# Optimization experiments

Measured on AMD Instinct MI355X. Metric: run time of the kernel, lower is better.

## Reference

```python
import jax, jax.numpy as jnp
from jax import lax
import numpy as np

B, T, D, H = 32, 512, 512, 1024  # batch, n_steps, in_channels (embedding), cell units


def setup_inputs() -> dict:
    key = jax.random.key(0)
    k1, k2, k3, k4 = jax.random.split(key, 4)
    inputs = jax.random.normal(k1, (B, T, D), dtype=jnp.float32)
    # actual (unpadded) length of each sequence, in [1, T]
    sequence_length = jax.random.randint(k2, (B,), 1, T + 1).astype(jnp.int32)
    # LSTMCell params: kernel [D, 4H], recurrent_kernel [H, 4H], bias [4H]; gate order i,f,g,o
    Wx = jax.random.normal(k3, (D, 4 * H), dtype=jnp.float32) * (1.0 / np.sqrt(D))
    Wh = jax.random.normal(k4, (H, 4 * H), dtype=jnp.float32) * (1.0 / np.sqrt(H))
    # unit_forget_bias=True: forget-gate bias initialized to 1
    b = jnp.concatenate([jnp.zeros((H,)), jnp.ones((H,)), jnp.zeros((2 * H,))]).astype(jnp.float32)
    return {"inputs": inputs, "sequence_length": sequence_length, "Wx": Wx, "Wh": Wh, "b": b}


def _lstm_all_outputs(inputs, Wx, Wh, b):
    # Precompute input projections for every timestep (big batched GEMM, fused).
    x_proj = jnp.einsum('btd,dk->btk', inputs, Wx) + b  # [B, T, 4H]

    def step(carry, xz_t):
        h, c = carry
        z = xz_t + h @ Wh  # [B, 4H]
        i, f, g, o = jnp.split(z, 4, axis=-1)
        i = jax.nn.sigmoid(i)
        f = jax.nn.sigmoid(f)
        o = jax.nn.sigmoid(o)
        c = f * c + i * jnp.tanh(g)
        h = o * jnp.tanh(c)
        return (h, c), h

    h0 = jnp.zeros((inputs.shape[0], Wh.shape[0]), dtype=inputs.dtype)
    c0 = h0
    (_, _), hs = lax.scan(step, (h0, c0), jnp.swapaxes(x_proj, 0, 1))  # hs: [T, B, H]
    return jnp.swapaxes(hs, 0, 1)  # [B, T, H]


def reference(inputs, sequence_length, Wx, Wh, b):
    # return_last_output=True with sequence_length: gather the output at the
    # actual last valid timestep (seq_len - 1) of each sequence.
    hs = _lstm_all_outputs(inputs, Wx, Wh, b)  # [B, T, H]
    last_idx = jnp.clip(sequence_length - 1, 0, inputs.shape[1] - 1)
    return hs[jnp.arange(hs.shape[0]), last_idx]  # [B, H]
```

## Files before the change

### kernel.cpp

```cpp
#include <hip/hip_runtime.h>
#include <hip/hip_bf16.h>


#define B_   32
#define T_   512
#define D_   512
#define H_   1024
#define KTOT 1536
#define N4H  4096
#define NBLK 64

typedef __bf16 bf16_t;
typedef __bf16 bf16x8 __attribute__((ext_vector_type(8)));
typedef float f32x4 __attribute__((ext_vector_type(4)));

#define MFMA16(a, b, c) __builtin_amdgcn_mfma_f32_16x16x32_bf16(a, b, c, 0, 0, 0)

__global__ void wconv_kernel(const float* __restrict__ Wx,
                             const float* __restrict__ Wh,
                             bf16_t* __restrict__ Wt) {
    __shared__ float tile[32][33];
    int k0 = blockIdx.x * 32;
    int n0 = blockIdx.y * 32;
    int tx = threadIdx.x;
    int ty = threadIdx.y;
    for (int i = ty; i < 32; i += 8) {
        int k = k0 + i;
        float v = (k < H_) ? Wh[(size_t)k * N4H + n0 + tx]
                           : Wx[(size_t)(k - H_) * N4H + n0 + tx];
        tile[i][tx] = v;
    }
    __syncthreads();
    for (int i = ty; i < 32; i += 8)
        Wt[(size_t)(n0 + i) * KTOT + k0 + tx] = (bf16_t)tile[tx][i];
}

__global__ void xconv_kernel(const float4* __restrict__ X,
                             uint4* __restrict__ Xpk) {
    int i = blockIdx.x * blockDim.x + threadIdx.x;
    float4 v = X[i];
    float arr[4] = {v.x, v.y, v.z, v.w};
    unsigned pk[4];
#pragma unroll
    for (int j = 0; j < 4; ++j) {
        bf16_t h = (bf16_t)arr[j];
        bf16_t l = (bf16_t)(arr[j] - (float)h);
        pk[j] = (unsigned)__builtin_bit_cast(unsigned short, h) |
                ((unsigned)__builtin_bit_cast(unsigned short, l) << 16);
    }
    Xpk[i] = make_uint4(pk[0], pk[1], pk[2], pk[3]);
}

__device__ __forceinline__ void unpack16(const unsigned short* s,
                                         bf16x8* hi, bf16x8* lo) {
#pragma unroll
    for (int j = 0; j < 8; ++j) {
        (*hi)[j] = __builtin_bit_cast(bf16_t, s[2 * j]);
        (*lo)[j] = __builtin_bit_cast(bf16_t, s[2 * j + 1]);
    }
}

__global__ __launch_bounds__(512, 2) void lstm_kernel(
    const bf16_t* __restrict__ Wt,
    const unsigned* __restrict__ Xpk,
    unsigned* __restrict__ hpk,
    const float* __restrict__ bias,
    const int* __restrict__ seqlen,
    float* __restrict__ out,
    unsigned* __restrict__ flags) {
    __shared__ float zpart[8][4][32][16];
    __shared__ unsigned stage[512];

    const int tid  = threadIdx.x;
    const int w    = tid >> 6;
    const int lane = tid & 63;
    const int quad = lane >> 4;
    const int lcol = lane & 15;
    const int hc0  = blockIdx.x * 16;
    const int HW_  = 32768;

    bf16x8 wreg[24];
#pragma unroll
    for (int g = 0; g < 4; ++g)
#pragma unroll
        for (int it = 0; it < 6; ++it) {
            int k = (it < 4) ? (w * 128 + it * 32)
                             : (1024 + w * 64 + (it - 4) * 32);
            wreg[g * 6 + it] = *(const bf16x8*)(
                Wt + (size_t)(g * H_ + hc0 + lcol) * KTOT + k + quad * 8);
        }

    const int eb = tid >> 4, ec = tid & 15;
    const int col = hc0 + ec;
    float creg = 0.f;
    const float b0 = bias[col];
    const float b1 = bias[H_ + col];
    const float b2 = bias[2 * H_ + col];
    const float b3 = bias[3 * H_ + col];
    const int slm1 = seqlen[eb] - 1;
    const int stageIdx = (eb >> 4) * 256 + ((ec >> 3) * 16 + (eb & 15)) * 8 +
                         (ec & 7);
    const int kbB  = (hc0 >> 5) * 1024;
    const int qlo  = (hc0 >> 4) & 1;
    const int QU   = (kbB >> 1) + qlo * 128;
    const int myflag = ((blockIdx.x >> 3) << 4) | (blockIdx.x & 7);
    const unsigned* pollp = flags + w * 16 + (lane & 7);

#pragma unroll 1
    for (int t = 0; t < T_; ++t) {
        const unsigned* hr = hpk + (size_t)(t & 1) * HW_;
        unsigned*       hw = hpk + (size_t)((t + 1) & 1) * HW_;

        f32x4 acc[8];
#pragma unroll
        for (int i = 0; i < 8; ++i) acc[i] = (f32x4){0.f, 0.f, 0.f, 0.f};

#pragma unroll
        for (int itx = 0; itx < 2; ++itx) {
            int kx = w * 64 + itx * 32 + quad * 8;
            union { uint4 q[2]; unsigned short s[16]; } u0, u1;
            const unsigned* p0 = Xpk + ((size_t)lcol * T_ + t) * D_ + kx;
            const unsigned* p1 = Xpk + ((size_t)(lcol + 16) * T_ + t) * D_ + kx;
            u0.q[0] = *(const uint4*)p0;
            u0.q[1] = *(const uint4*)(p0 + 4);
            u1.q[0] = *(const uint4*)p1;
            u1.q[1] = *(const uint4*)(p1 + 4);
            bf16x8 a0h, a0l, a1h, a1l;
            unpack16(u0.s, &a0h, &a0l);
            unpack16(u1.s, &a1h, &a1l);
#pragma unroll
            for (int g = 0; g < 4; ++g) {
                bf16x8 wv = wreg[g * 6 + 4 + itx];
                acc[g * 2]     = MFMA16(a0h, wv, acc[g * 2]);
                acc[g * 2]     = MFMA16(a0l, wv, acc[g * 2]);
                acc[g * 2 + 1] = MFMA16(a1h, wv, acc[g * 2 + 1]);
                acc[g * 2 + 1] = MFMA16(a1l, wv, acc[g * 2 + 1]);
            }
        }

        {
            const unsigned tgt = (unsigned)t;
            for (;;) {
                unsigned v = __hip_atomic_load(pollp, __ATOMIC_RELAXED,
                                               __HIP_MEMORY_SCOPE_AGENT);
                if (__all((int)(v >= tgt))) break;
            }
            asm volatile("" ::: "memory");
        }

        union Raw { unsigned long long u[4]; unsigned short s[16]; };
        Raw r[8];
#pragma unroll
        for (int it = 0; it < 4; ++it) {
            const unsigned long long* q = (const unsigned long long*)(
                hr + (w * 4 + it) * 1024 + lane * 8);
#pragma unroll
            for (int j = 0; j < 4; ++j)
                r[it * 2].u[j] = __hip_atomic_load(
                    q + j, __ATOMIC_RELAXED, __HIP_MEMORY_SCOPE_AGENT);
#pragma unroll
            for (int j = 0; j < 4; ++j)
                r[it * 2 + 1].u[j] = __hip_atomic_load(
                    q + 256 + j, __ATOMIC_RELAXED, __HIP_MEMORY_SCOPE_AGENT);
        }
#pragma unroll
        for (int it = 0; it < 4; ++it) {
            bf16x8 a0h, a0l, a1h, a1l;
            unpack16(r[it * 2].s, &a0h, &a0l);
            unpack16(r[it * 2 + 1].s, &a1h, &a1l);
#pragma unroll
            for (int g = 0; g < 4; ++g) {
                bf16x8 wv = wreg[g * 6 + it];
                acc[g * 2]     = MFMA16(a0h, wv, acc[g * 2]);
                acc[g * 2]     = MFMA16(a0l, wv, acc[g * 2]);
                acc[g * 2 + 1] = MFMA16(a1h, wv, acc[g * 2 + 1]);
                acc[g * 2 + 1] = MFMA16(a1l, wv, acc[g * 2 + 1]);
            }
        }

#pragma unroll
        for (int g = 0; g < 4; ++g)
#pragma unroll
            for (int r4 = 0; r4 < 4; ++r4) {
                zpart[w][g][quad * 4 + r4][lcol]      = acc[g * 2][r4];
                zpart[w][g][16 + quad * 4 + r4][lcol] = acc[g * 2 + 1][r4];
            }
        __syncthreads();

        float zi = b0, zf = b1, zg = b2, zo = b3;
#pragma unroll
        for (int ss = 0; ss < 8; ++ss) {
            zi += zpart[ss][0][eb][ec];
            zf += zpart[ss][1][eb][ec];
            zg += zpart[ss][2][eb][ec];
            zo += zpart[ss][3][eb][ec];
        }
        float ig = 1.f / (1.f + __expf(-zi));
        float fg = 1.f / (1.f + __expf(-zf));
        float og = 1.f / (1.f + __expf(-zo));
        float gg = 1.f - 2.f / (__expf(2.f * zg) + 1.f);
        creg = fg * creg + ig * gg;
        float hn = og * (1.f - 2.f / (__expf(2.f * creg) + 1.f));
        bf16_t hh = (bf16_t)hn;
        bf16_t hl = (bf16_t)(hn - (float)hh);
        unsigned pk = (unsigned)__builtin_bit_cast(unsigned short, hh) |
                      ((unsigned)__builtin_bit_cast(unsigned short, hl) << 16);
        stage[stageIdx] = pk;
        if (slm1 == t) out[eb * H_ + col] = hn;

        __syncthreads();

        if (w == 0) {
            const unsigned long long* sp = (const unsigned long long*)stage;
            unsigned long long* hwu = (unsigned long long*)hw;
#pragma unroll
            for (int j = 0; j < 4; ++j) {
                unsigned long long val = sp[j * 64 + lane];
                __hip_atomic_store(
                    hwu + QU + (j >> 1) * 256 + (j & 1) * 64 + lane, val,
                    __ATOMIC_RELAXED, __HIP_MEMORY_SCOPE_AGENT);
            }
            asm volatile("s_waitcnt vmcnt(0)" ::: "memory");
            if (lane == 0)
                __hip_atomic_store(flags + myflag, (unsigned)(t + 1),
                                   __ATOMIC_RELAXED, __HIP_MEMORY_SCOPE_AGENT);
        }
    }
}

extern "C" void kernel_launch(void* const* d_in, const int* in_sizes, int n_in,
                              void* d_out, int out_size, void* d_ws, size_t ws_size,
                              hipStream_t stream) {
    const float* inputs = (const float*)d_in[0];
    const int*   seqlen = (const int*)d_in[1];
    const float* Wx     = (const float*)d_in[2];
    const float* Wh     = (const float*)d_in[3];
    const float* bias   = (const float*)d_in[4];
    float* out = (float*)d_out;

    char* ws = (char*)d_ws;
    size_t o = 0;
    bf16_t*   Wt    = (bf16_t*)(ws + o);   o += (size_t)N4H * KTOT * 2;
    unsigned* Xpk   = (unsigned*)(ws + o); o += (size_t)B_ * T_ * D_ * 4;
    unsigned* hpk   = (unsigned*)(ws + o); o += (size_t)2 * B_ * H_ * 4;
    unsigned* flags = (unsigned*)(ws + o); o += 4096;

    wconv_kernel<<<dim3(48, 128), dim3(32, 8), 0, stream>>>(Wx, Wh, Wt);
    xconv_kernel<<<(B_ * T_ * D_ / 4) / 256, 256, 0, stream>>>(
        (const float4*)inputs, (uint4*)Xpk);
    hipMemsetAsync(hpk, 0, (size_t)B_ * H_ * 4, stream);
    hipMemsetAsync(flags, 0, 4096, stream);

    lstm_kernel<<<NBLK, 512, 0, stream>>>(Wt, Xpk, hpk, bias, seqlen, out, flags);
}
```

Baseline: 3.399 ms.

## Overlap input projection GEMM with recurrence via producer blocks and counters

Adds 192 producer blocks that compute the input projection x·Wx for pairs of timesteps into a global fp32 buffer. Each producer bumps a per-timestep-pair counter when its tile is stored. The 64 recurrent blocks poll that counter and load the precomputed gate inputs, so the per-step MFMA work over the input part of K is removed from the serial critical path. This costs a large workspace buffer, extra memory traffic, and the risk that producers compete with the recurrent blocks for CUs and bandwidth. Launch bounds drop to one block per CU, and if the workspace is too small the kernel falls back to the old path.

```diff
diff --git a/kernel.cpp b/kernel.cpp
--- a/kernel.cpp
+++ b/kernel.cpp
@@ -9,6 +9,8 @@
 #define KTOT 1536
 #define N4H  4096
 #define NBLK 64
+#define NPROD 192
+#define NITEM 16384
 
 typedef __bf16 bf16_t;
 typedef __bf16 bf16x8 __attribute__((ext_vector_type(8)));
@@ -60,14 +62,17 @@
     }
 }
 
-__global__ __launch_bounds__(512, 2) void lstm_kernel(
+template <int XP>
+__global__ __launch_bounds__(512, 1) void lstm_kernel(
     const bf16_t* __restrict__ Wt,
     const unsigned* __restrict__ Xpk,
+    float* __restrict__ xproj,
     unsigned* __restrict__ hpk,
     const float* __restrict__ bias,
     const int* __restrict__ seqlen,
     float* __restrict__ out,
-    unsigned* __restrict__ flags) {
+    unsigned* __restrict__ flags,
+    unsigned* __restrict__ counters) {
     __shared__ float zpart[8][4][32][16];
     __shared__ unsigned stage[512];
 
@@ -76,19 +81,82 @@
     const int lane = tid & 63;
     const int quad = lane >> 4;
     const int lcol = lane & 15;
-    const int hc0  = blockIdx.x * 16;
-    const int HW_  = 32768;
-
-    bf16x8 wreg[24];
-#pragma unroll
-    for (int g = 0; g < 4; ++g)
-#pragma unroll
-        for (int it = 0; it < 6; ++it) {
-            int k = (it < 4) ? (w * 128 + it * 32)
-                             : (1024 + w * 64 + (it - 4) * 32);
-            wreg[g * 6 + it] = *(const bf16x8*)(
-                Wt + (size_t)(g * H_ + hc0 + lcol) * KTOT + k + quad * 8);
-        }
+
+    if (XP && (int)blockIdx.x >= NBLK) {
+#pragma unroll 1
+        for (int item = (int)blockIdx.x - NBLK; item < NITEM; item += NPROD) {
+            const int tt = item >> 6;
+            const int nt = item & 63;
+            const int m0 = tt * 64 + (w >> 2) * 32;
+            const int n0 = nt * 64 + (w & 3) * 16;
+            const int t0 = tt * 2;
+            bf16x8 wr[16];
+#pragma unroll
+            for (int kk = 0; kk < 16; ++kk)
+                wr[kk] = *(const bf16x8*)(Wt + (size_t)(n0 + lcol) * KTOT +
+                                          1024 + kk * 32 + quad * 8);
+            f32x4 acc0 = {0.f, 0.f, 0.f, 0.f};
+            f32x4 acc1 = {0.f, 0.f, 0.f, 0.f};
+#pragma unroll 4
+            for (int kk = 0; kk < 16; ++kk) {
+                union { uint4 q[2]; unsigned short s[16]; } u0, u1;
+                const unsigned* p0 =
+                    Xpk + ((size_t)lcol * T_ + t0) * D_ + kk * 32 + quad * 8;
+                const unsigned* p1 =
+                    Xpk + ((size_t)lcol * T_ + t0 + 1) * D_ + kk * 32 + quad * 8;
+                u0.q[0] = *(const uint4*)p0;
+                u0.q[1] = *(const uint4*)(p0 + 4);
+                u1.q[0] = *(const uint4*)p1;
+                u1.q[1] = *(const uint4*)(p1 + 4);
+                bf16x8 a0h, a0l, a1h, a1l;
+                unpack16(u0.s, &a0h, &a0l);
+                unpack16(u1.s, &a1h, &a1l);
+                acc0 = MFMA16(a0h, wr[kk], acc0);
+                acc0 = MFMA16(a0l, wr[kk], acc0);
+                acc1 = MFMA16(a1h, wr[kk], acc1);
+                acc1 = MFMA16(a1l, wr[kk], acc1);
+            }
+#pragma unroll
+            for (int r = 0; r < 4; ++r) {
+                __hip_atomic_store(
+                    xproj + (size_t)(m0 + quad * 4 + r) * N4H + n0 + lcol,
+                    acc0[r], __ATOMIC_RELAXED, __HIP_MEMORY_SCOPE_AGENT);
+                __hip_atomic_store(
+                    xproj + (size_t)(m0 + 32 + quad * 4 + r) * N4H + n0 + lcol,
+                    acc1[r], __ATOMIC_RELAXED, __HIP_MEMORY_SCOPE_AGENT);
+            }
+            asm volatile("s_waitcnt vmcnt(0)" ::: "memory");
+            __syncthreads();
+            if (tid == 0)
+                __hip_atomic_fetch_add(counters + tt, 1u, __ATOMIC_RELAXED,
+                                       __HIP_MEMORY_SCOPE_AGENT);
+        }
+        return;
+    }
+
+    const int hc0 = blockIdx.x * 16;
+    const int HW_ = 32768;
+
+    bf16x8 wreg[XP ? 16 : 24];
+    if (XP) {
+#pragma unroll
+        for (int g = 0; g < 4; ++g)
+#pragma unroll
+            for (int it = 0; it < 4; ++it)
+                wreg[g * 4 + it] = *(const bf16x8*)(
+                    Wt + (size_t)(g * H_ + hc0 + lcol) * KTOT + w * 128 +
+                    it * 32 + quad * 8);
+    } else {
+#pragma unroll
+        for (int g = 0; g < 4; ++g)
+#pragma unroll
+            for (int it = 0; it < 6; ++it) {
+                int k = (it < 4) ? (w * 128 + it * 32)
+                                 : (1024 + w * 64 + (it - 4) * 32);
+                wreg[g * 6 + it] = *(const bf16x8*)(
+                    Wt + (size_t)(g * H_ + hc0 + lcol) * KTOT + k + quad * 8);
+            }
+    }
 
     const int eb = tid >> 4, ec = tid & 15;
     const int col = hc0 + ec;
@@ -115,26 +183,48 @@
 #pragma unroll
         for (int i = 0; i < 8; ++i) acc[i] = (f32x4){0.f, 0.f, 0.f, 0.f};
 
-#pragma unroll
-        for (int itx = 0; itx < 2; ++itx) {
-            int kx = w * 64 + itx * 32 + quad * 8;
-            union { uint4 q[2]; unsigned short s[16]; } u0, u1;
-            const unsigned* p0 = Xpk + ((size_t)lcol * T_ + t) * D_ + kx;
-            const unsigned* p1 = Xpk + ((size_t)(lcol + 16) * T_ + t) * D_ + kx;
-            u0.q[0] = *(const uint4*)p0;
-            u0.q[1] = *(const uint4*)(p0 + 4);
-            u1.q[0] = *(const uint4*)p1;
-            u1.q[1] = *(const uint4*)(p1 + 4);
-            bf16x8 a0h, a0l, a1h, a1l;
-            unpack16(u0.s, &a0h, &a0l);
-            unpack16(u1.s, &a1h, &a1l);
-#pragma unroll
-            for (int g = 0; g < 4; ++g) {
-                bf16x8 wv = wreg[g * 6 + 4 + itx];
-                acc[g * 2]     = MFMA16(a0h, wv, acc[g * 2]);
-                acc[g * 2]     = MFMA16(a0l, wv, acc[g * 2]);
-                acc[g * 2 + 1] = MFMA16(a1h, wv, acc[g * 2 + 1]);
-                acc[g * 2 + 1] = MFMA16(a1l, wv, acc[g * 2 + 1]);
+        float xp0, xp1, xp2, xp3;
+        if (XP) {
+            if ((t & 1) == 0) {
+                const unsigned* cp = counters + (t >> 1);
+                while (__hip_atomic_load(cp, __ATOMIC_RELAXED,
+                                         __HIP_MEMORY_SCOPE_AGENT) < 64u)
+                    __builtin_amdgcn_s_sleep(1);
+            }
+            asm volatile("" ::: "memory");
+            const float* xpt = xproj + (size_t)(t * B_ + eb) * N4H + col;
+            xp0 = __hip_atomic_load(xpt, __ATOMIC_RELAXED,
+                                    __HIP_MEMORY_SCOPE_AGENT);
+            xp1 = __hip_atomic_load(xpt + H_, __ATOMIC_RELAXED,
+                                    __HIP_MEMORY_SCOPE_AGENT);
+            xp2 = __hip_atomic_load(xpt + 2 * H_, __ATOMIC_RELAXED,
+                                    __HIP_MEMORY_SCOPE_AGENT);
+            xp3 = __hip_atomic_load(xpt + 3 * H_, __ATOMIC_RELAXED,
+                                    __HIP_MEMORY_SCOPE_AGENT);
+        } else {
+            xp0 = xp1 = xp2 = xp3 = 0.f;
+#pragma unroll
+            for (int itx = 0; itx < 2; ++itx) {
+                int kx = w * 64 + itx * 32 + quad * 8;
+                union { uint4 q[2]; unsigned short s[16]; } u0, u1;
+                const unsigned* p0 = Xpk + ((size_t)lcol * T_ + t) * D_ + kx;
+                const unsigned* p1 =
+                    Xpk + ((size_t)(lcol + 16) * T_ + t) * D_ + kx;
+                u0.q[0] = *(const uint4*)p0;
+                u0.q[1] = *(const uint4*)(p0 + 4);
+                u1.q[0] = *(const uint4*)p1;
+                u1.q[1] = *(const uint4*)(p1 + 4);
+                bf16x8 a0h, a0l, a1h, a1l;
+                unpack16(u0.s, &a0h, &a0l);
+                unpack16(u1.s, &a1h, &a1l);
+#pragma unroll
+                for (int g = 0; g < 4; ++g) {
+                    bf16x8 wv = wreg[g * 6 + 4 + itx];
+                    acc[g * 2]     = MFMA16(a0h, wv, acc[g * 2]);
+                    acc[g * 2]     = MFMA16(a0l, wv, acc[g * 2]);
+                    acc[g * 2 + 1] = MFMA16(a1h, wv, acc[g * 2 + 1]);
+                    acc[g * 2 + 1] = MFMA16(a1l, wv, acc[g * 2 + 1]);
+                }
             }
         }
 
@@ -170,7 +260,7 @@
             unpack16(r[it * 2 + 1].s, &a1h, &a1l);
 #pragma unroll
             for (int g = 0; g < 4; ++g) {
-                bf16x8 wv = wreg[g * 6 + it];
+                bf16x8 wv = XP ? wreg[g * 4 + it] : wreg[g * 6 + it];
                 acc[g * 2]     = MFMA16(a0h, wv, acc[g * 2]);
                 acc[g * 2]     = MFMA16(a0l, wv, acc[g * 2]);
                 acc[g * 2 + 1] = MFMA16(a1h, wv, acc[g * 2 + 1]);
@@ -187,7 +277,7 @@
             }
         __syncthreads();
 
-        float zi = b0, zf = b1, zg = b2, zo = b3;
+        float zi = b0 + xp0, zf = b1 + xp1, zg = b2 + xp2, zo = b3 + xp3;
 #pragma unroll
         for (int ss = 0; ss < 8; ++ss) {
             zi += zpart[ss][0][eb][ec];
@@ -244,12 +334,21 @@
     unsigned* Xpk   = (unsigned*)(ws + o); o += (size_t)B_ * T_ * D_ * 4;
     unsigned* hpk   = (unsigned*)(ws + o); o += (size_t)2 * B_ * H_ * 4;
     unsigned* flags = (unsigned*)(ws + o); o += 4096;
+    unsigned* cnts  = (unsigned*)(ws + o); o += 4096;
+    float*    xproj = (float*)(ws + o);
+    const size_t NEED = o + (size_t)B_ * T_ * N4H * 4;
+    const bool use_xp = ws_size >= NEED;
 
     wconv_kernel<<<dim3(48, 128), dim3(32, 8), 0, stream>>>(Wx, Wh, Wt);
     xconv_kernel<<<(B_ * T_ * D_ / 4) / 256, 256, 0, stream>>>(
         (const float4*)inputs, (uint4*)Xpk);
     hipMemsetAsync(hpk, 0, (size_t)B_ * H_ * 4, stream);
-    hipMemsetAsync(flags, 0, 4096, stream);
-
-    lstm_kernel<<<NBLK, 512, 0, stream>>>(Wt, Xpk, hpk, bias, seqlen, out, flags);
-}
+    hipMemsetAsync(flags, 0, 8192, stream);
+
+    if (use_xp)
+        lstm_kernel<1><<<NBLK + NPROD, 512, 0, stream>>>(
+            Wt, Xpk, xproj, hpk, bias, seqlen, out, flags, cnts);
+    else
+        lstm_kernel<0><<<NBLK, 512, 0, stream>>>(
+            Wt, Xpk, xproj, hpk, bias, seqlen, out, flags, cnts);
+}
```

After: 3.413 ms. About the same (+0.4%).

## Use per-timestep hidden-state slots so h reads become plain vector loads

Applied to the files above, without the earlier changes.

Replaces the two-slot ping-pong hidden-state buffer with 513 distinct slots, one per timestep, written in descending address order, whenever the workspace is large enough. Every address is then written only once, so no stale cached copy can exist and the h reads can use ordinary 128-bit vector loads instead of per-qword relaxed agent-scope atomic loads. Launch bounds are also relaxed to one block per CU, which gives the compiler more registers. In exchange it needs about 64MB more workspace and keeps a fallback path. It also relies on plain loads not hitting stale cache lines, which holds only because the write-once pattern guarantees it.

```diff
diff --git a/kernel.cpp b/kernel.cpp
--- a/kernel.cpp
+++ b/kernel.cpp
@@ -9,6 +9,7 @@
 #define KTOT 1536
 #define N4H  4096
 #define NBLK 64
+#define NSLOT 513
 
 typedef __bf16 bf16_t;
 typedef __bf16 bf16x8 __attribute__((ext_vector_type(8)));
@@ -60,7 +61,8 @@
     }
 }
 
-__global__ __launch_bounds__(512, 2) void lstm_kernel(
+template <int XP>
+__global__ __launch_bounds__(512, 1) void lstm_kernel(
     const bf16_t* __restrict__ Wt,
     const unsigned* __restrict__ Xpk,
     unsigned* __restrict__ hpk,
@@ -108,8 +110,8 @@
 
 #pragma unroll 1
     for (int t = 0; t < T_; ++t) {
-        const unsigned* hr = hpk + (size_t)(t & 1) * HW_;
-        unsigned*       hw = hpk + (size_t)((t + 1) & 1) * HW_;
+        const unsigned* hr = hpk + (size_t)(XP ? (512 - t) : (t & 1)) * HW_;
+        unsigned*       hw = hpk + (size_t)(XP ? (511 - t) : ((t + 1) & 1)) * HW_;
 
         f32x4 acc[8];
 #pragma unroll
@@ -148,20 +150,32 @@
             asm volatile("" ::: "memory");
         }
 
-        union Raw { unsigned long long u[4]; unsigned short s[16]; };
+        union Raw { uint4 q[2]; unsigned long long u[4]; unsigned short s[16]; };
         Raw r[8];
-#pragma unroll
-        for (int it = 0; it < 4; ++it) {
-            const unsigned long long* q = (const unsigned long long*)(
-                hr + (w * 4 + it) * 1024 + lane * 8);
-#pragma unroll
-            for (int j = 0; j < 4; ++j)
-                r[it * 2].u[j] = __hip_atomic_load(
-                    q + j, __ATOMIC_RELAXED, __HIP_MEMORY_SCOPE_AGENT);
-#pragma unroll
-            for (int j = 0; j < 4; ++j)
-                r[it * 2 + 1].u[j] = __hip_atomic_load(
-                    q + 256 + j, __ATOMIC_RELAXED, __HIP_MEMORY_SCOPE_AGENT);
+        if (XP) {
+#pragma unroll
+            for (int it = 0; it < 4; ++it) {
+                const uint4* q =
+                    (const uint4*)(hr + (w * 4 + it) * 1024 + lane * 8);
+                r[it * 2].q[0]     = q[0];
+                r[it * 2].q[1]     = q[1];
+                r[it * 2 + 1].q[0] = q[128];
+                r[it * 2 + 1].q[1] = q[129];
+            }
+        } else {
+#pragma unroll
+            for (int it = 0; it < 4; ++it) {
+                const unsigned long long* q = (const unsigned long long*)(
+                    hr + (w * 4 + it) * 1024 + lane * 8);
+#pragma unroll
+                for (int j = 0; j < 4; ++j)
+                    r[it * 2].u[j] = __hip_atomic_load(
+                        q + j, __ATOMIC_RELAXED, __HIP_MEMORY_SCOPE_AGENT);
+#pragma unroll
+                for (int j = 0; j < 4; ++j)
+                    r[it * 2 + 1].u[j] = __hip_atomic_load(
+                        q + 256 + j, __ATOMIC_RELAXED, __HIP_MEMORY_SCOPE_AGENT);
+            }
         }
 #pragma unroll
         for (int it = 0; it < 4; ++it) {
@@ -242,14 +256,23 @@
     size_t o = 0;
     bf16_t*   Wt    = (bf16_t*)(ws + o);   o += (size_t)N4H * KTOT * 2;
     unsigned* Xpk   = (unsigned*)(ws + o); o += (size_t)B_ * T_ * D_ * 4;
-    unsigned* hpk   = (unsigned*)(ws + o); o += (size_t)2 * B_ * H_ * 4;
     unsigned* flags = (unsigned*)(ws + o); o += 4096;
+    unsigned* hpk   = (unsigned*)(ws + o);
+    const size_t slotB = (size_t)B_ * H_ * 4;
+    const size_t NEED  = o + (size_t)NSLOT * slotB;
+    const bool use_xp  = ws_size >= NEED;
 
     wconv_kernel<<<dim3(48, 128), dim3(32, 8), 0, stream>>>(Wx, Wh, Wt);
     xconv_kernel<<<(B_ * T_ * D_ / 4) / 256, 256, 0, stream>>>(
         (const float4*)inputs, (uint4*)Xpk);
-    hipMemsetAsync(hpk, 0, (size_t)B_ * H_ * 4, stream);
     hipMemsetAsync(flags, 0, 4096, stream);
-
-    lstm_kernel<<<NBLK, 512, 0, stream>>>(Wt, Xpk, hpk, bias, seqlen, out, flags);
-}
+    if (use_xp) {
+        hipMemsetAsync(hpk + (size_t)512 * B_ * H_, 0, slotB, stream);
+        lstm_kernel<1><<<NBLK, 512, 0, stream>>>(Wt, Xpk, hpk, bias, seqlen,
+                                                 out, flags);
+    } else {
+        hipMemsetAsync(hpk, 0, slotB, stream);
+        lstm_kernel<0><<<NBLK, 512, 0, stream>>>(Wt, Xpk, hpk, bias, seqlen,
+                                                 out, flags);
+    }
+}
```

Result: faster. 2.726 ms (-19.8%).
